# Optimization experiments

Measured on AMD Instinct MI355X. Metric: run time of the kernel, lower is better.

The kernel has to match this reference:

```python
import jax, jax.numpy as jnp
import numpy as np
import itertools

N_BITS = 64   # data_info['n']
K_MAX = 3     # data_info['k']
BATCH = 8192


def _build_table(n, k):
    # All 0/1 vectors of length n with at most k ones, ordered by popcount then lexicographic
    rows = [np.zeros((1, n), dtype=np.int32)]
    for i in range(1, k + 1):
        idxs = np.array(list(itertools.combinations(range(n), i)), dtype=np.int64)  # (C(n,i), i)
        t = np.zeros((idxs.shape[0], n), dtype=np.int32)
        t[np.arange(idxs.shape[0])[:, None], idxs] = 1
        rows.append(t)
    return np.concatenate(rows, axis=0)  # (total_case, n)


def setup_inputs() -> dict:
    key = jax.random.key(0)
    table_np = _build_table(N_BITS, K_MAX)
    total_case = table_np.shape[0]  # 43745 for n=64, k=3
    k1, k2 = jax.random.split(key)
    # x must exactly match a table row (original code's .nonzero()[0] assumes a match exists)
    sel = jax.random.randint(k1, (BATCH,), 0, total_case)
    table = jnp.asarray(table_np)
    x = table[sel]  # (BATCH, n) int32, each row has <= k ones
    W = jax.random.normal(k2, (total_case,), dtype=jnp.float32)
    return {"x": x, "table": table, "W": W}


def reference(x, table, W):
    # Original per-sample loop: idx_i = first row r with sum(table[r] ^ x_i) == 0.
    # For 0/1 vectors, sum(a ^ b) = sum(a) + sum(b) - 2 * (a . b), so the whole
    # batch reduces to one GEMM + an equality test + argmax (first True).
    xf = x.astype(jnp.float32)
    tf = table.astype(jnp.float32)
    xs = jnp.sum(xf, axis=1)          # (B,)
    ts = jnp.sum(tf, axis=1)          # (T,)
    dot = xf @ tf.T                   # (B, T)
    mismatch = xs[:, None] + ts[None, :] - 2.0 * dot  # (B, T) popcount of XOR
    idx = jnp.argmax(mismatch == 0.0, axis=1)         # first exact match per row
    logw = jnp.log(jax.nn.softmax(W))                 # matches torch: log(softmax(W))
    return logw[idx]                                  # (B,)
```

## Files before the change

kernel.cpp:

```cpp
#include <hip/hip_runtime.h>

__global__ void partial_exp_kernel(const float* __restrict__ W, int T,
                                   float* __restrict__ partials) {
    __shared__ float red[4];
    const int tid  = threadIdx.x;
    const int lane = tid & 63;
    const int wave = tid >> 6;
    float s = 0.0f;
    for (int i = blockIdx.x * blockDim.x + tid; i < T; i += gridDim.x * blockDim.x)
        s += expf(W[i]);
    for (int off = 32; off > 0; off >>= 1) s += __shfl_down(s, off, 64);
    if (lane == 0) red[wave] = s;
    __syncthreads();
    if (tid == 0)
        partials[blockIdx.x] = red[0] + red[1] + red[2] + red[3];
}

__global__ void rank_kernel(const int* __restrict__ x,
                            const float* __restrict__ W,
                            const float* __restrict__ partials,
                            float* __restrict__ out, int batch) {
    const int lane = threadIdx.x & 63;
    const int row  = (int)((blockIdx.x * blockDim.x + threadIdx.x) >> 6);
    if (row >= batch) return;

    float p = (lane < 32) ? partials[lane] : 0.0f;
    for (int off = 32; off > 0; off >>= 1) p += __shfl_down(p, off, 64);

    const int v = x[row * 64 + lane];
    const unsigned long long mask = __ballot(v != 0);
    if (lane == 0) {
        const int m = __popcll(mask);
        int idx;
        if (m == 0) {
            idx = 0;
        } else {
            unsigned long long t = mask;
            const int a = __builtin_ctzll(t); t &= t - 1;
            if (m == 1) {
                idx = 1 + a;
            } else {
                const int b = __builtin_ctzll(t); t &= t - 1;
                if (m == 2) {
                    idx = 65 + ((4032 - (63 - a) * (64 - a)) >> 1) + (b - a - 1);
                } else {
                    const int c = __builtin_ctzll(t);
                    const int s1 = 41664 - ((64 - a) * (63 - a) * (62 - a)) / 6;
                    const int s2 = ((62 - a) * (63 - a) - (63 - b) * (64 - b)) >> 1;
                    idx = 2081 + s1 + s2 + (c - b - 1);
                }
            }
        }
        out[row] = W[idx] - logf(p);
    }
}

extern "C" void kernel_launch(void* const* d_in, const int* in_sizes, int n_in,
                              void* d_out, int out_size, void* d_ws, size_t ws_size,
                              hipStream_t stream) {
    const int*   x = (const int*)d_in[0];
    const float* W = (const float*)d_in[2];
    float* out      = (float*)d_out;
    float* partials = (float*)d_ws;

    const int T = in_sizes[2];
    const int B = in_sizes[0] / 64;

    partial_exp_kernel<<<32, 256, 0, stream>>>(W, T, partials);

    const int threads = 256;
    const int rows_per_block = threads / 64;
    const int blocks = (B + rows_per_block - 1) / rows_per_block;
    rank_kernel<<<blocks, threads, 0, stream>>>(x, W, partials, out, B);
}
```

Baseline: 67.24 us.

## Fuse softmax normalizer and index lookup into one kernel with redundant per-block reduction

```diff
diff --git a/kernel.cpp b/kernel.cpp
--- a/kernel.cpp
+++ b/kernel.cpp
@@ -1,57 +1,57 @@
 #include <hip/hip_runtime.h>
 
-__global__ void partial_exp_kernel(const float* __restrict__ W, int T,
-                                   float* __restrict__ partials) {
-    __shared__ float red[4];
+__global__ __launch_bounds__(1024) void fused_kernel(
+        const int* __restrict__ x,
+        const float* __restrict__ W,
+        float* __restrict__ out,
+        int T, int batch) {
+    __shared__ float red[16];
     const int tid  = threadIdx.x;
     const int lane = tid & 63;
     const int wave = tid >> 6;
+
     float s = 0.0f;
-    for (int i = blockIdx.x * blockDim.x + tid; i < T; i += gridDim.x * blockDim.x)
-        s += expf(W[i]);
+    for (int i = tid; i < T; i += 1024) s += expf(W[i]);
     for (int off = 32; off > 0; off >>= 1) s += __shfl_down(s, off, 64);
     if (lane == 0) red[wave] = s;
     __syncthreads();
-    if (tid == 0)
-        partials[blockIdx.x] = red[0] + red[1] + red[2] + red[3];
-}
+    float tot = 0.0f;
+    #pragma unroll
+    for (int i = 0; i < 16; i++) tot += red[i];
+    const float lse = logf(tot);
 
-__global__ void rank_kernel(const int* __restrict__ x,
-                            const float* __restrict__ W,
-                            const float* __restrict__ partials,
-                            float* __restrict__ out, int batch) {
-    const int lane = threadIdx.x & 63;
-    const int row  = (int)((blockIdx.x * blockDim.x + threadIdx.x) >> 6);
-    if (row >= batch) return;
-
-    float p = (lane < 32) ? partials[lane] : 0.0f;
-    for (int off = 32; off > 0; off >>= 1) p += __shfl_down(p, off, 64);
-
-    const int v = x[row * 64 + lane];
-    const unsigned long long mask = __ballot(v != 0);
-    if (lane == 0) {
-        const int m = __popcll(mask);
-        int idx;
-        if (m == 0) {
-            idx = 0;
-        } else {
-            unsigned long long t = mask;
-            const int a = __builtin_ctzll(t); t &= t - 1;
-            if (m == 1) {
-                idx = 1 + a;
+    const int rows_per_block = (batch + gridDim.x - 1) / gridDim.x;
+    const int rows_per_wave  = (rows_per_block + 15) / 16;
+    const int row0 = blockIdx.x * rows_per_block + wave * rows_per_wave;
+    for (int r = 0; r < rows_per_wave; r++) {
+        const int row = row0 + r;
+        if (row >= batch) break;
+        const int v = x[row * 64 + lane];
+        const unsigned long long mask = __ballot(v != 0);
+        if (lane == 0) {
+            const int m = __popcll(mask);
+            int idx;
+            if (m == 0) {
+                idx = 0;
             } else {
-                const int b = __builtin_ctzll(t); t &= t - 1;
-                if (m == 2) {
-                    idx = 65 + ((4032 - (63 - a) * (64 - a)) >> 1) + (b - a - 1);
+                unsigned long long t = mask;
+                const int a = __builtin_ctzll(t); t &= t - 1;
+                if (m == 1) {
+                    idx = 1 + a;
                 } else {
-                    const int c = __builtin_ctzll(t);
-                    const int s1 = 41664 - ((64 - a) * (63 - a) * (62 - a)) / 6;
-                    const int s2 = ((62 - a) * (63 - a) - (63 - b) * (64 - b)) >> 1;
-                    idx = 2081 + s1 + s2 + (c - b - 1);
+                    const int b = __builtin_ctzll(t); t &= t - 1;
+                    if (m == 2) {
+                        idx = 65 + ((4032 - (63 - a) * (64 - a)) >> 1) + (b - a - 1);
+                    } else {
+                        const int c = __builtin_ctzll(t);
+                        const int s1 = 41664 - ((64 - a) * (63 - a) * (62 - a)) / 6;
+                        const int s2 = ((62 - a) * (63 - a) - (63 - b) * (64 - b)) >> 1;
+                        idx = 2081 + s1 + s2 + (c - b - 1);
+                    }
                 }
             }
+            out[row] = W[idx] - lse;
         }
-        out[row] = W[idx] - logf(p);
     }
 }
 
@@ -60,16 +60,10 @@
                               hipStream_t stream) {
     const int*   x = (const int*)d_in[0];
     const float* W = (const float*)d_in[2];
-    float* out      = (float*)d_out;
-    float* partials = (float*)d_ws;
+    float* out = (float*)d_out;
 
     const int T = in_sizes[2];
     const int B = in_sizes[0] / 64;
 
-    partial_exp_kernel<<<32, 256, 0, stream>>>(W, T, partials);
-
-    const int threads = 256;
-    const int rows_per_block = threads / 64;
-    const int blocks = (B + rows_per_block - 1) / rows_per_block;
-    rank_kernel<<<blocks, threads, 0, stream>>>(x, W, partials, out, B);
+    fused_kernel<<<256, 1024, 0, stream>>>(x, W, out, T, B);
 }
```

Result: slower. 76.19 us (+13.3%).
